# Optimization experiments

Hardware: AMD Instinct MI355X
Metric: run time of the kernel (lower is better)

The kernel has to match this reference:

```python
import jax, jax.numpy as jnp
import numpy as np

E, D, H, N = 16, 1024, 4096, 16384  # experts, idim, hidden_units, total tokens


def setup_inputs() -> dict:
    key = jax.random.key(0)
    k1, k2, k3, k4, k5 = jax.random.split(key, 5)
    s1 = 1.0 / np.sqrt(D)  # kaiming-uniform-ish bound for fan_in=D
    s2 = 1.0 / np.sqrt(H)
    return {
        "xs": jax.random.normal(k1, (N, D), dtype=jnp.float32),
        # tokens are grouped contiguously per expert; uniform load here
        "fwd_expert_count": jnp.full((E,), N // E, dtype=jnp.int32),
        "w1": jax.random.uniform(k2, (E, H, D), jnp.float32, -s1, s1),
        "b1": jax.random.uniform(k3, (E, H), jnp.float32, -s1, s1),
        "w2": jax.random.uniform(k4, (E, D, H), jnp.float32, -s2, s2),
        "b2": jax.random.uniform(k5, (E, D), jnp.float32, -s2, s2),
    }


def reference(xs, fwd_expert_count, w1, b1, w2, b2):
    # Grouped GEMM expert FFN (FMoELinear -> ReLU -> FMoELinear).
    # Counts are uniform (N//E per expert), so the per-expert grouped GEMM
    # is exactly a batched matmul over the expert axis.
    x = xs.reshape(E, N // E, D)                       # [E, n, D]
    h = jnp.einsum('end,ehd->enh', x, w1) + b1[:, None, :]  # [E, n, H]
    h = jax.nn.relu(h)                                 # dropout_rate=0 -> identity
    y = jnp.einsum('enh,edh->end', h, w2) + b2[:, None, :]  # [E, n, D]
    return y.reshape(N, D)
```

## Files before the change

kernel.cpp:

```cpp
#include <hip/hip_runtime.h>

#define E_  16
#define D_  1024
#define H_  4096
#define NPE 1024

typedef __bf16 bf16x8 __attribute__((ext_vector_type(8)));
typedef float f32x4 __attribute__((ext_vector_type(4)));

__device__ __forceinline__ unsigned short f2bf(float f) {
  unsigned int u = __float_as_uint(f);
  u += 0x7fffu + ((u >> 16) & 1u);
  return (unsigned short)(u >> 16);
}

__global__ __launch_bounds__(256) void cvt_f32_to_bf16(
    const float* __restrict__ in, unsigned short* __restrict__ out, int nvec) {
  const int stride = gridDim.x * 256;
#pragma unroll 4
  for (int i = blockIdx.x * 256 + threadIdx.x; i < nvec; i += stride) {
    float4 v = ((const float4*)in)[i];
    ushort4 o;
    o.x = f2bf(v.x);
    o.y = f2bf(v.y);
    o.z = f2bf(v.z);
    o.w = f2bf(v.w);
    ((ushort4*)out)[i] = o;
  }
}

__device__ __forceinline__ void wg_barrier() {
  asm volatile("" ::: "memory");
  __builtin_amdgcn_s_barrier();
  asm volatile("" ::: "memory");
}

template <bool RELU_BF16_OUT>
__global__ __launch_bounds__(512, 2) void gemm_bt(
    const unsigned short* __restrict__ A,
    const unsigned short* __restrict__ B,
    const float* __restrict__ bias,
    void* __restrict__ Cout,
    int M, int N, int K) {
  __shared__ __attribute__((aligned(16))) unsigned short ldsA[4 * 256 * 32];
  __shared__ __attribute__((aligned(16))) unsigned short ldsB[4 * 256 * 32];

  const int tid  = threadIdx.x;
  const int lane = tid & 63;
  const int wave = tid >> 6;
  const int wm   = wave >> 2;
  const int wn   = wave & 3;
  const int fr   = lane & 15;
  const int fq   = lane >> 4;

  const int Mt = M >> 8;
  const int Nt = N >> 8;
  const int id     = blockIdx.x;
  const int region = id & 7;
  const int slot   = id >> 3;
  const int bpe    = Mt * Nt;
  const int eloc   = slot / bpe;
  const int rem    = slot - eloc * bpe;
  const int e      = region * (E_ / 8) + eloc;
  const int SN     = Nt < 2 ? Nt : 2;
  const int csz    = Mt * SN;
  const int chunk  = rem / csz;
  const int inner  = rem - chunk * csz;
  const int mt     = inner % Mt;
  const int nt     = chunk * SN + inner / Mt;

  const int bm = mt << 8;
  const int bn = nt << 8;

  const unsigned short* Ae = A + (size_t)e * M * K;
  const unsigned short* Be = B + (size_t)e * N * K;

  const int srow   = lane >> 2;
  const int schunk = (lane & 3) ^ ((lane >> 3) & 3);
  const size_t aSrc0 = (size_t)(bm + wave * 16 + srow) * K + schunk * 8;
  const size_t aSrc1 = (size_t)(bm + 128 + wave * 16 + srow) * K + schunk * 8;
  const size_t bSrc0 = (size_t)(bn + wave * 16 + srow) * K + schunk * 8;
  const size_t bSrc1 = (size_t)(bn + 128 + wave * 16 + srow) * K + schunk * 8;

#define STAGE(KT)                                                              \
  do {                                                                         \
    const int _bo = ((KT) & 3) * 8192 + wave * 512;                            \
    const size_t _k = (size_t)(KT) << 5;                                       \
    __builtin_amdgcn_global_load_lds((const unsigned int*)(Ae + aSrc0 + _k),   \
                                     (unsigned int*)(ldsA + _bo), 16, 0, 0);   \
    __builtin_amdgcn_global_load_lds((const unsigned int*)(Ae + aSrc1 + _k),   \
                                     (unsigned int*)(ldsA + _bo + 4096), 16, 0, 0); \
    __builtin_amdgcn_global_load_lds((const unsigned int*)(Be + bSrc0 + _k),   \
                                     (unsigned int*)(ldsB + _bo), 16, 0, 0);   \
    __builtin_amdgcn_global_load_lds((const unsigned int*)(Be + bSrc1 + _k),   \
                                     (unsigned int*)(ldsB + _bo + 4096), 16, 0, 0); \
  } while (0)

  const int swz   = (fq ^ ((fr >> 1) & 3)) << 3;
  const int abase = (wm * 128 + fr) * 32 + swz;
  const int bbase = (wn * 64 + fr) * 32 + swz;

  f32x4 acc[8][4];
  const f32x4 zero = {0.f, 0.f, 0.f, 0.f};
#pragma unroll
  for (int i = 0; i < 8; ++i)
#pragma unroll
    for (int j = 0; j < 4; ++j) acc[i][j] = zero;

  const int nK = K >> 5;
  STAGE(0);
  if (nK > 1) STAGE(1);
  if (nK > 2) STAGE(2);

#pragma unroll 1
  for (int kt = 0; kt < nK; ++kt) {
    if (kt + 3 < nK) STAGE(kt + 3);
    asm volatile("s_waitcnt vmcnt(12)" ::: "memory");
    wg_barrier();

    const unsigned short* lA = ldsA + (kt & 3) * 8192;
    const unsigned short* lB = ldsB + (kt & 3) * 8192;

    bf16x8 a0[4], a1[4], b0[4];
#pragma unroll
    for (int i = 0; i < 4; ++i) a0[i] = *(const bf16x8*)&lA[abase + i * 512];
#pragma unroll
    for (int i = 0; i < 4; ++i) b0[i] = *(const bf16x8*)&lB[bbase + i * 512];
#pragma unroll
    for (int i = 0; i < 4; ++i)
      a1[i] = *(const bf16x8*)&lA[abase + 2048 + i * 512];

    __builtin_amdgcn_s_setprio(1);
#pragma unroll
    for (int mi = 0; mi < 4; ++mi)
#pragma unroll
      for (int ni = 0; ni < 4; ++ni)
        acc[mi][ni] = __builtin_amdgcn_mfma_f32_16x16x32_bf16(
            a0[mi], b0[ni], acc[mi][ni], 0, 0, 0);
#pragma unroll
    for (int mi = 0; mi < 4; ++mi)
#pragma unroll
      for (int ni = 0; ni < 4; ++ni)
        acc[4 + mi][ni] = __builtin_amdgcn_mfma_f32_16x16x32_bf16(
            a1[mi], b0[ni], acc[4 + mi][ni], 0, 0, 0);
    __builtin_amdgcn_s_setprio(0);
    wg_barrier();
  }
#undef STAGE

  const int crow0 = bm + wm * 128 + fq * 4;
  const int ccol0 = bn + wn * 64 + fr;
  float bv[4];
#pragma unroll
  for (int ni = 0; ni < 4; ++ni) bv[ni] = bias[(size_t)e * N + ccol0 + ni * 16];

  if (RELU_BF16_OUT) {
    unsigned short* C = (unsigned short*)Cout + (size_t)e * M * N;
#pragma unroll
    for (int mi = 0; mi < 8; ++mi)
#pragma unroll
      for (int ni = 0; ni < 4; ++ni)
#pragma unroll
        for (int r = 0; r < 4; ++r) {
          float v = acc[mi][ni][r] + bv[ni];
          v = v > 0.f ? v : 0.f;
          C[(size_t)(crow0 + mi * 16 + r) * N + ccol0 + ni * 16] = f2bf(v);
        }
  } else {
    float* C = (float*)Cout + (size_t)e * M * N;
#pragma unroll
    for (int mi = 0; mi < 8; ++mi)
#pragma unroll
      for (int ni = 0; ni < 4; ++ni)
#pragma unroll
        for (int r = 0; r < 4; ++r) {
          C[(size_t)(crow0 + mi * 16 + r) * N + ccol0 + ni * 16] =
              acc[mi][ni][r] + bv[ni];
        }
  }
}

extern "C" void kernel_launch(void* const* d_in, const int* in_sizes, int n_in,
                              void* d_out, int out_size, void* d_ws, size_t ws_size,
                              hipStream_t stream) {
  (void)in_sizes; (void)n_in; (void)out_size; (void)ws_size;
  const float* xs = (const float*)d_in[0];
  const float* w1 = (const float*)d_in[2];
  const float* b1 = (const float*)d_in[3];
  const float* w2 = (const float*)d_in[4];
  const float* b2 = (const float*)d_in[5];
  float* y = (float*)d_out;

  char* ws = (char*)d_ws;
  unsigned short* xs_bf = (unsigned short*)ws;
  unsigned short* w_bf  = (unsigned short*)(ws + (size_t)(32u << 20));
  unsigned short* h_bf  = (unsigned short*)(ws + (size_t)(160u << 20));

  const int nXs = E_ * NPE * D_;
  const int nW  = E_ * H_ * D_;

  cvt_f32_to_bf16<<<2048, 256, 0, stream>>>(xs, xs_bf, nXs / 4);
  cvt_f32_to_bf16<<<2048, 256, 0, stream>>>(w1, w_bf, nW / 4);

  gemm_bt<true><<<E_ * (NPE / 256) * (H_ / 256), 512, 0, stream>>>(
      xs_bf, w_bf, b1, h_bf, NPE, H_, D_);

  cvt_f32_to_bf16<<<2048, 256, 0, stream>>>(w2, w_bf, nW / 4);

  gemm_bt<false><<<E_ * (NPE / 256) * (D_ / 256), 512, 0, stream>>>(
      h_bf, w_bf, b2, y, NPE, D_, H_);
}
```

Baseline: 1.003 ms.

## Template GEMM tile height, switch to double buffering, unroll conversion loop

The GEMM kernel now takes the M tile height as a template parameter, so the second GEMM uses 128-row tiles and launches twice as many workgroups. The four-stage LDS ring with vmcnt(12) is replaced by a two-buffer scheme that waits for all loads before each barrier and then issues the next stage. LDS use drops, and the conversion kernel is manually unrolled with four independent loads per iteration. The shallower prefetch exposes more global-load latency per k-step. In exchange, the smaller footprint could raise occupancy and the extra blocks improve load balance for the second GEMM.

```diff
diff --git a/kernel.cpp b/kernel.cpp
--- a/kernel.cpp
+++ b/kernel.cpp
@@ -14,19 +14,32 @@
   return (unsigned short)(u >> 16);
 }
 
+__device__ __forceinline__ ushort4 cvt4(float4 v) {
+  ushort4 o;
+  o.x = f2bf(v.x);
+  o.y = f2bf(v.y);
+  o.z = f2bf(v.z);
+  o.w = f2bf(v.w);
+  return o;
+}
+
 __global__ __launch_bounds__(256) void cvt_f32_to_bf16(
     const float* __restrict__ in, unsigned short* __restrict__ out, int nvec) {
   const int stride = gridDim.x * 256;
-#pragma unroll 4
-  for (int i = blockIdx.x * 256 + threadIdx.x; i < nvec; i += stride) {
-    float4 v = ((const float4*)in)[i];
-    ushort4 o;
-    o.x = f2bf(v.x);
-    o.y = f2bf(v.y);
-    o.z = f2bf(v.z);
-    o.w = f2bf(v.w);
-    ((ushort4*)out)[i] = o;
-  }
+  int i = blockIdx.x * 256 + threadIdx.x;
+  const int nmain = nvec - 3 * stride;
+  for (; i < nmain; i += 4 * stride) {
+    float4 v0 = ((const float4*)in)[i];
+    float4 v1 = ((const float4*)in)[i + stride];
+    float4 v2 = ((const float4*)in)[i + 2 * stride];
+    float4 v3 = ((const float4*)in)[i + 3 * stride];
+    ((ushort4*)out)[i]              = cvt4(v0);
+    ((ushort4*)out)[i + stride]     = cvt4(v1);
+    ((ushort4*)out)[i + 2 * stride] = cvt4(v2);
+    ((ushort4*)out)[i + 3 * stride] = cvt4(v3);
+  }
+  for (; i < nvec; i += stride)
+    ((ushort4*)out)[i] = cvt4(((const float4*)in)[i]);
 }
 
 __device__ __forceinline__ void wg_barrier() {
@@ -35,15 +48,18 @@
   asm volatile("" ::: "memory");
 }
 
-template <bool RELU_BF16_OUT>
+template <int BM, bool RELU_BF16_OUT>
 __global__ __launch_bounds__(512, 2) void gemm_bt(
     const unsigned short* __restrict__ A,
     const unsigned short* __restrict__ B,
     const float* __restrict__ bias,
     void* __restrict__ Cout,
     int M, int N, int K) {
-  __shared__ __attribute__((aligned(16))) unsigned short ldsA[4 * 256 * 32];
-  __shared__ __attribute__((aligned(16))) unsigned short ldsB[4 * 256 * 32];
+  constexpr int BN    = 256;
+  constexpr int MR    = BM / 32;
+  constexpr int LOADS = (BM + BN) / 128;
+  constexpr int BUFE  = (BM + BN) * 32;
+  __shared__ __attribute__((aligned(16))) unsigned short lds[2][BUFE];
 
   const int tid  = threadIdx.x;
   const int lane = tid & 63;
@@ -53,7 +69,7 @@
   const int fr   = lane & 15;
   const int fq   = lane >> 4;
 
-  const int Mt = M >> 8;
+  const int Mt = M / BM;
   const int Nt = N >> 8;
   const int id     = blockIdx.x;
   const int region = id & 7;
@@ -69,86 +85,77 @@
   const int mt     = inner % Mt;
   const int nt     = chunk * SN + inner / Mt;
 
-  const int bm = mt << 8;
+  const int bm = mt * BM;
   const int bn = nt << 8;
 
   const unsigned short* Ae = A + (size_t)e * M * K;
   const unsigned short* Be = B + (size_t)e * N * K;
 
-  const int srow   = lane >> 2;
-  const int schunk = (lane & 3) ^ ((lane >> 3) & 3);
-  const size_t aSrc0 = (size_t)(bm + wave * 16 + srow) * K + schunk * 8;
-  const size_t aSrc1 = (size_t)(bm + 128 + wave * 16 + srow) * K + schunk * 8;
-  const size_t bSrc0 = (size_t)(bn + wave * 16 + srow) * K + schunk * 8;
-  const size_t bSrc1 = (size_t)(bn + 128 + wave * 16 + srow) * K + schunk * 8;
-
-#define STAGE(KT)                                                              \
+  const unsigned short* gsrc[LOADS];
+  unsigned short* l0[LOADS];
+#pragma unroll
+  for (int t = 0; t < LOADS; ++t) {
+    const int c   = t * 512 + tid;
+    const bool isA = c < BM * 4;
+    const int cl  = isA ? c : c - BM * 4;
+    const int r   = cl >> 2;
+    const int q   = (cl & 3) ^ ((r >> 1) & 3);
+    gsrc[t] = (isA ? Ae + (size_t)(bm + r) * K : Be + (size_t)(bn + r) * K) + q * 8;
+    l0[t]   = &lds[0][0] + t * 4096 + wave * 512;
+  }
+
+#define STAGE(KT, BUF)                                                         \
   do {                                                                         \
-    const int _bo = ((KT) & 3) * 8192 + wave * 512;                            \
+    const int _bs = (BUF) * BUFE;                                              \
     const size_t _k = (size_t)(KT) << 5;                                       \
-    __builtin_amdgcn_global_load_lds((const unsigned int*)(Ae + aSrc0 + _k),   \
-                                     (unsigned int*)(ldsA + _bo), 16, 0, 0);   \
-    __builtin_amdgcn_global_load_lds((const unsigned int*)(Ae + aSrc1 + _k),   \
-                                     (unsigned int*)(ldsA + _bo + 4096), 16, 0, 0); \
-    __builtin_amdgcn_global_load_lds((const unsigned int*)(Be + bSrc0 + _k),   \
-                                     (unsigned int*)(ldsB + _bo), 16, 0, 0);   \
-    __builtin_amdgcn_global_load_lds((const unsigned int*)(Be + bSrc1 + _k),   \
-                                     (unsigned int*)(ldsB + _bo + 4096), 16, 0, 0); \
+    _Pragma("unroll")                                                          \
+    for (int t = 0; t < LOADS; ++t)                                            \
+      __builtin_amdgcn_global_load_lds((const unsigned int*)(gsrc[t] + _k),    \
+                                       (unsigned int*)(l0[t] + _bs), 16, 0, 0);\
   } while (0)
 
-  const int swz   = (fq ^ ((fr >> 1) & 3)) << 3;
-  const int abase = (wm * 128 + fr) * 32 + swz;
-  const int bbase = (wn * 64 + fr) * 32 + swz;
-
-  f32x4 acc[8][4];
+  const int swz  = (fq ^ ((fr >> 1) & 3)) << 3;
+  const int aoff = (wm * (BM / 2) + fr) * 32 + swz;
+  const int boff = BM * 32 + (wn * 64 + fr) * 32 + swz;
+
+  f32x4 acc[MR][4];
   const f32x4 zero = {0.f, 0.f, 0.f, 0.f};
 #pragma unroll
-  for (int i = 0; i < 8; ++i)
+  for (int i = 0; i < MR; ++i)
 #pragma unroll
     for (int j = 0; j < 4; ++j) acc[i][j] = zero;
 
   const int nK = K >> 5;
-  STAGE(0);
-  if (nK > 1) STAGE(1);
-  if (nK > 2) STAGE(2);
+  STAGE(0, 0);
+  int buf = 0;
 
 #pragma unroll 1
   for (int kt = 0; kt < nK; ++kt) {
-    if (kt + 3 < nK) STAGE(kt + 3);
-    asm volatile("s_waitcnt vmcnt(12)" ::: "memory");
+    asm volatile("s_waitcnt vmcnt(0)" ::: "memory");
     wg_barrier();
-
-    const unsigned short* lA = ldsA + (kt & 3) * 8192;
-    const unsigned short* lB = ldsB + (kt & 3) * 8192;
-
-    bf16x8 a0[4], a1[4], b0[4];
-#pragma unroll
-    for (int i = 0; i < 4; ++i) a0[i] = *(const bf16x8*)&lA[abase + i * 512];
-#pragma unroll
-    for (int i = 0; i < 4; ++i) b0[i] = *(const bf16x8*)&lB[bbase + i * 512];
-#pragma unroll
-    for (int i = 0; i < 4; ++i)
-      a1[i] = *(const bf16x8*)&lA[abase + 2048 + i * 512];
+    if (kt + 1 < nK) STAGE(kt + 1, buf ^ 1);
+
+    const unsigned short* L = &lds[0][0] + buf * BUFE;
+    bf16x8 af[MR], bfv[4];
+#pragma unroll
+    for (int i = 0; i < MR; ++i) af[i] = *(const bf16x8*)&L[aoff + i * 512];
+#pragma unroll
+    for (int i = 0; i < 4; ++i) bfv[i] = *(const bf16x8*)&L[boff + i * 512];
 
     __builtin_amdgcn_s_setprio(1);
 #pragma unroll
-    for (int mi = 0; mi < 4; ++mi)
+    for (int mi = 0; mi < MR; ++mi)
 #pragma unroll
       for (int ni = 0; ni < 4; ++ni)
         acc[mi][ni] = __builtin_amdgcn_mfma_f32_16x16x32_bf16(
-            a0[mi], b0[ni], acc[mi][ni], 0, 0, 0);
-#pragma unroll
-    for (int mi = 0; mi < 4; ++mi)
-#pragma unroll
-      for (int ni = 0; ni < 4; ++ni)
-        acc[4 + mi][ni] = __builtin_amdgcn_mfma_f32_16x16x32_bf16(
-            a1[mi], b0[ni], acc[4 + mi][ni], 0, 0, 0);
+            af[mi], bfv[ni], acc[mi][ni], 0, 0, 0);
     __builtin_amdgcn_s_setprio(0);
     wg_barrier();
+    buf ^= 1;
   }
 #undef STAGE
 
-  const int crow0 = bm + wm * 128 + fq * 4;
+  const int crow0 = bm + wm * (BM / 2) + fq * 4;
   const int ccol0 = bn + wn * 64 + fr;
   float bv[4];
 #pragma unroll
@@ -157,7 +164,7 @@
   if (RELU_BF16_OUT) {
     unsigned short* C = (unsigned short*)Cout + (size_t)e * M * N;
 #pragma unroll
-    for (int mi = 0; mi < 8; ++mi)
+    for (int mi = 0; mi < MR; ++mi)
 #pragma unroll
       for (int ni = 0; ni < 4; ++ni)
 #pragma unroll
@@ -169,7 +176,7 @@
   } else {
     float* C = (float*)Cout + (size_t)e * M * N;
 #pragma unroll
-    for (int mi = 0; mi < 8; ++mi)
+    for (int mi = 0; mi < MR; ++mi)
 #pragma unroll
       for (int ni = 0; ni < 4; ++ni)
 #pragma unroll
@@ -202,11 +209,11 @@
   cvt_f32_to_bf16<<<2048, 256, 0, stream>>>(xs, xs_bf, nXs / 4);
   cvt_f32_to_bf16<<<2048, 256, 0, stream>>>(w1, w_bf, nW / 4);
 
-  gemm_bt<true><<<E_ * (NPE / 256) * (H_ / 256), 512, 0, stream>>>(
+  gemm_bt<256, true><<<E_ * (NPE / 256) * (H_ / 256), 512, 0, stream>>>(
       xs_bf, w_bf, b1, h_bf, NPE, H_, D_);
 
   cvt_f32_to_bf16<<<2048, 256, 0, stream>>>(w2, w_bf, nW / 4);
 
-  gemm_bt<false><<<E_ * (NPE / 256) * (D_ / 256), 512, 0, stream>>>(
+  gemm_bt<128, false><<<E_ * (NPE / 128) * (D_ / 256), 512, 0, stream>>>(
       h_bf, w_bf, b2, y, NPE, D_, H_);
 }
```

Measured after the change: 951.9 us. 1.05x faster.
